# Kernel optimization log

Measured on AMD Instinct MI355X. Metric: run time of the kernel, lower is better.

The kernel has to match this reference:

```python
import jax, jax.numpy as jnp
import numpy as np

D_MODEL = 768
NUM_HEAD = 12
D_K = D_MODEL // NUM_HEAD
NEG_BIG = -1e9


def setup_inputs() -> dict:
    key = jax.random.key(0)
    ks = jax.random.split(key, 16)
    B, S, D = 16, 512, D_MODEL
    scale = 1.0 / np.sqrt(D)
    inp = {
        "q": jax.random.normal(ks[0], (B, S, D), jnp.float32),
        "k": jax.random.normal(ks[1], (B, S, D), jnp.float32),
        "v": jax.random.normal(ks[2], (B, S, D), jnp.float32),
        # padding mask: 1 where masked, broadcast over heads and query dim
        "mask": jax.random.randint(ks[3], (B, 1, 1, S), 0, 2).astype(jnp.float32),
        # adjacency bias broadcast over heads
        "adj": jax.random.uniform(ks[4], (B, 1, S, S), jnp.float32),
        "Wq": jax.random.normal(ks[5], (D, D), jnp.float32) * scale,
        "bq": jnp.zeros((D,), jnp.float32),
        "Wk": jax.random.normal(ks[6], (D, D), jnp.float32) * scale,
        "bk": jnp.zeros((D,), jnp.float32),
        "Wv": jax.random.normal(ks[7], (D, D), jnp.float32) * scale,
        "bv": jnp.zeros((D,), jnp.float32),
        "Wo": jax.random.normal(ks[8], (D, D), jnp.float32) * scale,
        "bo": jnp.zeros((D,), jnp.float32),
    }
    return inp


def reference(q, k, v, mask, adj, Wq, bq, Wk, bk, Wv, bv, Wo, bo):
    B, S, D = q.shape
    H, dk = NUM_HEAD, D_K

    def proj(x, W, b):
        # nn.Linear: x @ W.T + b, then split heads -> [B, H, S, dk]
        y = jnp.einsum('bsd,ed->bse', x, W) + b
        return y.reshape(B, S, H, dk).transpose(0, 2, 1, 3)

    qh = proj(q, Wq, bq)
    kh = proj(k, Wk, bk)
    vh = proj(v, Wv, bv)

    scores = jnp.einsum('bhqd,bhkd->bhqk', qh, kh) / jnp.sqrt(jnp.float32(dk))
    scores = scores + mask * NEG_BIG + adj  # broadcast over heads
    attn = jax.nn.softmax(scores, axis=-1)
    x = jnp.einsum('bhqk,bhkd->bhqd', attn, vh)
    x = x.transpose(0, 2, 1, 3).reshape(B, S, D)
    return jnp.einsum('bsd,ed->bse', x, Wo) + bo
```

## Files before the change

### kernel.cpp

```cpp
#include <hip/hip_runtime.h>
#include <hip/hip_bf16.h>

#define SEQ 512
#define DM 768
#define NH 12
#define DK 64
#define NB 16
#define WN (DM * DM)
#define HE ((size_t)NB * SEQ * DM)

typedef __attribute__((ext_vector_type(8))) _Float16 f16x8;
typedef __attribute__((ext_vector_type(4))) float f32x4;

static __device__ __forceinline__ void gload16(const void* g, void* lds) {
    __builtin_amdgcn_global_load_lds(
        (const __attribute__((address_space(1))) unsigned int*)g,
        (__attribute__((address_space(3))) unsigned int*)lds, 16, 0, 0);
}

__global__ __launch_bounds__(256) void convert_w(
    const float* __restrict__ Wq, const float* __restrict__ Wk,
    const float* __restrict__ Wv, const float* __restrict__ Wo,
    _Float16* __restrict__ dst)
{
    size_t i8 = ((size_t)blockIdx.x * 256 + threadIdx.x) * 8;
    unsigned int s = (unsigned int)(i8 / WN);
    const float* src = s == 0 ? Wq : s == 1 ? Wk : s == 2 ? Wv : Wo;
    size_t off = i8 - (size_t)s * WN;
    float4 a = *(const float4*)(src + off);
    float4 b = *(const float4*)(src + off + 4);
    f16x8 h;
    h[0] = (_Float16)a.x; h[1] = (_Float16)a.y; h[2] = (_Float16)a.z; h[3] = (_Float16)a.w;
    h[4] = (_Float16)b.x; h[5] = (_Float16)b.y; h[6] = (_Float16)b.z; h[7] = (_Float16)b.w;
    *(f16x8*)(dst + i8) = h;
}

__global__ __launch_bounds__(256) void proj_qkv(
    const float* __restrict__ Aq, const float* __restrict__ Ak,
    const float* __restrict__ Av, const _Float16* __restrict__ Wh,
    const float* __restrict__ bq, const float* __restrict__ bk, const float* __restrict__ bv,
    _Float16* __restrict__ P1, _Float16* __restrict__ P2, _Float16* __restrict__ P3)
{
    __shared__ float As[128][64];
    __shared__ _Float16 Bs[128][64];
    const int f = blockIdx.x;
    const int lg = (f & 7) * 144 + (f >> 3);
    const int sel = lg / 384;
    const int rem = lg - sel * 384;
    const int bm = (rem / 6) * 128, bn = (rem % 6) * 128;
    const float* A = sel == 0 ? Aq : sel == 1 ? Ak : Av;
    const _Float16* W = Wh + (size_t)sel * WN;
    const float* bias = sel == 0 ? bq : sel == 1 ? bk : bv;
    _Float16* O = sel == 0 ? P1 : sel == 1 ? P2 : P3;

    const int t = threadIdx.x, lane = t & 63, w = t >> 6;
    const int wm = w >> 1, wn = w & 1, g = lane >> 4, r16 = lane & 15;

    const int ar4 = lane >> 4, agr = lane & 15;
    const int br8 = lane >> 3, bgr = lane & 7;

    f32x4 acc[4][4] = {};

    const _Float16* gbs = W + (size_t)(bn + w * 32 + br8) * DM + ((bgr ^ br8) * 8);

    for (int kk = 0; kk < DM; kk += 64) {
        #pragma unroll
        for (int j = 0; j < 8; ++j) {
            const int row = w * 32 + j * 4 + ar4;
            const int gg  = (agr & 8) + ((agr & 7) ^ (row & 7));
            gload16(A + (size_t)(bm + row) * DM + kk + gg * 4, &As[w * 32 + j * 4][0]);
        }
        #pragma unroll
        for (int j = 0; j < 4; ++j)
            gload16(gbs + kk + (size_t)j * 8 * DM, &Bs[w * 32 + j * 8][0]);
        __syncthreads();
        #pragma unroll
        for (int h = 0; h < 2; ++h) {
            f16x8 af[4], bf[4];
            #pragma unroll
            for (int mi = 0; mi < 4; ++mi) {
                const int row = wm * 64 + mi * 16 + r16;
                const int p0 = h * 8 + ((2 * g)     ^ (r16 & 7));
                const int p1 = h * 8 + ((2 * g + 1) ^ (r16 & 7));
                f32x4 x0 = *(f32x4*)&As[row][p0 * 4];
                f32x4 x1 = *(f32x4*)&As[row][p1 * 4];
                f16x8 hh;
                hh[0] = (_Float16)x0[0]; hh[1] = (_Float16)x0[1];
                hh[2] = (_Float16)x0[2]; hh[3] = (_Float16)x0[3];
                hh[4] = (_Float16)x1[0]; hh[5] = (_Float16)x1[1];
                hh[6] = (_Float16)x1[2]; hh[7] = (_Float16)x1[3];
                af[mi] = hh;
            }
            #pragma unroll
            for (int ni = 0; ni < 4; ++ni)
                bf[ni] = *(f16x8*)&Bs[wn * 64 + ni * 16 + r16][(((h * 4 + g) ^ (r16 & 7))) * 8];
            #pragma unroll
            for (int mi = 0; mi < 4; ++mi)
                #pragma unroll
                for (int ni = 0; ni < 4; ++ni)
                    acc[mi][ni] = __builtin_amdgcn_mfma_f32_16x16x32_f16(af[mi], bf[ni], acc[mi][ni], 0, 0, 0);
        }
        __syncthreads();
    }
    #pragma unroll
    for (int ni = 0; ni < 4; ++ni) {
        int n = bn + wn * 64 + ni * 16 + r16;
        float bv_ = bias[n];
        #pragma unroll
        for (int mi = 0; mi < 4; ++mi) {
            #pragma unroll
            for (int r = 0; r < 4; ++r) {
                int m = bm + wm * 64 + mi * 16 + g * 4 + r;
                O[(size_t)m * DM + n] = (_Float16)(acc[mi][ni][r] + bv_);
            }
        }
    }
}

__global__ __launch_bounds__(256) void proj_o(
    const _Float16* __restrict__ A, const _Float16* __restrict__ W,
    const float* __restrict__ bias, float* __restrict__ O32)
{
    __shared__ _Float16 As[128][64];
    __shared__ _Float16 Bs[128][64];
    const int f = blockIdx.x;
    const int lg = (f & 7) * 48 + (f >> 3);
    const int bm = (lg / 6) * 128, bn = (lg % 6) * 128;
    const int t = threadIdx.x, lane = t & 63, w = t >> 6;
    const int wm = w >> 1, wn = w & 1, g = lane >> 4, r16 = lane & 15;
    const int br8 = lane >> 3, bgr = lane & 7;

    f32x4 acc[4][4] = {};

    const _Float16* gas = A + (size_t)(bm + w * 32 + br8) * DM + ((bgr ^ br8) * 8);
    const _Float16* gbs = W + (size_t)(bn + w * 32 + br8) * DM + ((bgr ^ br8) * 8);

    for (int kk = 0; kk < DM; kk += 64) {
        #pragma unroll
        for (int j = 0; j < 4; ++j) {
            gload16(gas + kk + (size_t)j * 8 * DM, &As[w * 32 + j * 8][0]);
            gload16(gbs + kk + (size_t)j * 8 * DM, &Bs[w * 32 + j * 8][0]);
        }
        __syncthreads();
        #pragma unroll
        for (int h = 0; h < 2; ++h) {
            f16x8 af[4], bf[4];
            #pragma unroll
            for (int mi = 0; mi < 4; ++mi)
                af[mi] = *(f16x8*)&As[wm * 64 + mi * 16 + r16][((h * 4 + g) ^ (r16 & 7)) * 8];
            #pragma unroll
            for (int ni = 0; ni < 4; ++ni)
                bf[ni] = *(f16x8*)&Bs[wn * 64 + ni * 16 + r16][((h * 4 + g) ^ (r16 & 7)) * 8];
            #pragma unroll
            for (int mi = 0; mi < 4; ++mi)
                #pragma unroll
                for (int ni = 0; ni < 4; ++ni)
                    acc[mi][ni] = __builtin_amdgcn_mfma_f32_16x16x32_f16(af[mi], bf[ni], acc[mi][ni], 0, 0, 0);
        }
        __syncthreads();
    }
    #pragma unroll
    for (int ni = 0; ni < 4; ++ni) {
        int n = bn + wn * 64 + ni * 16 + r16;
        float bv_ = bias[n];
        #pragma unroll
        for (int mi = 0; mi < 4; ++mi) {
            #pragma unroll
            for (int r = 0; r < 4; ++r) {
                int m = bm + wm * 64 + mi * 16 + g * 4 + r;
                O32[(size_t)m * DM + n] = acc[mi][ni][r] + bv_;
            }
        }
    }
}

#define VSWI(d, kcol) ((d) * 72 + ((((kcol) * 2) ^ ((((d) >> 3) & 7) << 4)) >> 1))
__global__ __launch_bounds__(256) void attn(
    const _Float16* __restrict__ Qp, const _Float16* __restrict__ Kp,
    const _Float16* __restrict__ Vp, const float* __restrict__ Adj,
    const float* __restrict__ Mask, _Float16* __restrict__ X)
{
    __shared__ _Float16 Ks[2][64 * 64];
    __shared__ _Float16 Vt[2][64 * 72];
    __shared__ _Float16 Ps[4][16][72];
    const int id = blockIdx.x;
    const int lid = (id & 7) * 192 + (id >> 3);
    const int h = lid % NH, qb = (lid / NH) & 7, b = lid / (NH * 8);
    const int t = threadIdx.x, lane = t & 63, w = t >> 6;
    const int g = lane >> 4, r16 = lane & 15;
    const int srow = t >> 2, sc = (t & 3) * 16;

    const _Float16* Qg = Qp + (size_t)(b * SEQ + qb * 64 + w * 16 + r16) * DM + h * DK;
    const f16x8 qf0 = *(const f16x8*)(Qg + g * 8);
    const f16x8 qf1 = *(const f16x8*)(Qg + 32 + g * 8);

    const _Float16* Kbh   = Kp + (size_t)(b * SEQ) * DM + h * DK;
    const _Float16* Vbase = Vp + (size_t)(b * SEQ) * DM + h * DK + sc;
    const float* Abase = Adj + ((size_t)b << 18)
                             + (size_t)(qb * 64 + w * 16 + g * 4) * SEQ + r16;
    const float* Mbase = Mask + ((size_t)b << 9) + r16;

    uint4 vv[2];
    float am[16];
    float mtv[4];

#define STAGEK(KB, BUF) { _Pragma("unroll") for (int j_ = 0; j_ < 2; ++j_) { \
        const _Float16* src_ = Kbh + (size_t)((KB) * 64 + w * 16 + j_ * 8 + (lane >> 3)) * DM \
                              + (((lane & 7) ^ (lane >> 3)) * 8); \
        gload16(src_, &Ks[BUF][(w * 16 + j_ * 8) * 64]); } }
#define LOADV(KB) { const _Float16* vp_ = Vbase + (size_t)((KB) * 64 + srow) * DM; \
        vv[0] = ((const uint4*)vp_)[0]; vv[1] = ((const uint4*)vp_)[1]; }
#define LOADA(KB) { _Pragma("unroll") for (int r = 0; r < 4; ++r) \
        _Pragma("unroll") for (int cb = 0; cb < 4; ++cb) \
            am[r * 4 + cb] = Abase[(size_t)r * SEQ + (KB) * 64 + cb * 16]; \
        _Pragma("unroll") for (int cb = 0; cb < 4; ++cb) \
            mtv[cb] = Mbase[(KB) * 64 + cb * 16]; }

    STAGEK(0, 0);
    __builtin_amdgcn_sched_barrier(0);
    LOADV(0);
    LOADA(0);

    float l_lane[4] = {0.f, 0.f, 0.f, 0.f};
    f32x4 o[4] = {};

    #pragma unroll
    for (int kb = 0; kb < 8; ++kb) {
        const int buf = kb & 1;
        {
            union { uint4 u[2]; _Float16 hh[16]; } cv;
            cv.u[0] = vv[0]; cv.u[1] = vv[1];
            _Float16* vt = &Vt[buf][0];
            #pragma unroll
            for (int i = 0; i < 16; ++i) vt[VSWI(sc + i, srow)] = cv.hh[i];
        }
        asm volatile("s_waitcnt lgkmcnt(0)" ::: "memory");
        __builtin_amdgcn_sched_barrier(0);
        __builtin_amdgcn_s_barrier();
        __builtin_amdgcn_sched_barrier(0);

        f32x4 sf[4] = {};
        __builtin_amdgcn_s_setprio(1);
        #pragma unroll
        for (int cb = 0; cb < 4; ++cb) {
            const int R = cb * 16 + r16;
            f16x8 k0 = *(f16x8*)&Ks[buf][R * 64 + ((g ^ (r16 & 7)) * 8)];
            f16x8 k1 = *(f16x8*)&Ks[buf][R * 64 + (((4 + g) ^ (r16 & 7)) * 8)];
            sf[cb] = __builtin_amdgcn_mfma_f32_16x16x32_f16(qf0, k0, sf[cb], 0, 0, 0);
            sf[cb] = __builtin_amdgcn_mfma_f32_16x16x32_f16(qf1, k1, sf[cb], 0, 0, 0);
        }
        __builtin_amdgcn_s_setprio(0);
        if (kb < 7) {
            STAGEK(kb + 1, buf ^ 1);
            __builtin_amdgcn_sched_barrier(0);
            LOADV(kb + 1);
        }
        #pragma unroll
        for (int cb = 0; cb < 4; ++cb) {
            const float term = fmaf(mtv[cb], -43280.8512f, -11.54156036f);
            #pragma unroll
            for (int r = 0; r < 4; ++r) {
                float e = exp2f(fmaf(sf[cb][r], 0.18033688f,
                            fmaf(am[r * 4 + cb], 1.44269504f, term)));
                sf[cb][r] = e;
                l_lane[r] += e;
            }
        }
        if (kb < 7) LOADA(kb + 1);
        #pragma unroll
        for (int cb = 0; cb < 4; ++cb)
            #pragma unroll
            for (int r = 0; r < 4; ++r)
                Ps[w][g * 4 + r][cb * 16 + r16] = (_Float16)sf[cb][r];
        __builtin_amdgcn_s_setprio(1);
        #pragma unroll
        for (int ks = 0; ks < 2; ++ks) {
            f16x8 pf = *(f16x8*)&Ps[w][r16][ks * 32 + g * 8];
            #pragma unroll
            for (int db = 0; db < 4; ++db) {
                f16x8 vf = *(f16x8*)&Vt[buf][VSWI(db * 16 + r16, ks * 32 + g * 8)];
                o[db] = __builtin_amdgcn_mfma_f32_16x16x32_f16(pf, vf, o[db], 0, 0, 0);
            }
        }
        __builtin_amdgcn_s_setprio(0);
    }
#undef STAGEK
#undef LOADV
#undef LOADA
    #pragma unroll
    for (int d = 1; d < 16; d <<= 1)
        #pragma unroll
        for (int r = 0; r < 4; ++r)
            l_lane[r] += __shfl_xor(l_lane[r], d);
    const int qrow = qb * 64 + w * 16 + g * 4;
    #pragma unroll
    for (int r = 0; r < 4; ++r) {
        float inv = 1.f / l_lane[r];
        _Float16* xp = X + (size_t)(b * SEQ + qrow + r) * DM + h * DK;
        #pragma unroll
        for (int db = 0; db < 4; ++db)
            xp[db * 16 + r16] = (_Float16)(o[db][r] * inv);
    }
}

extern "C" void kernel_launch(void* const* d_in, const int* in_sizes, int n_in,
                              void* d_out, int out_size, void* d_ws, size_t ws_size,
                              hipStream_t stream)
{
    const float* q    = (const float*)d_in[0];
    const float* k    = (const float*)d_in[1];
    const float* v    = (const float*)d_in[2];
    const float* mask = (const float*)d_in[3];
    const float* adj  = (const float*)d_in[4];
    const float* Wq   = (const float*)d_in[5];
    const float* bq   = (const float*)d_in[6];
    const float* Wk   = (const float*)d_in[7];
    const float* bk   = (const float*)d_in[8];
    const float* Wv   = (const float*)d_in[9];
    const float* bv   = (const float*)d_in[10];
    const float* Wo   = (const float*)d_in[11];
    const float* bo   = (const float*)d_in[12];
    float* out = (float*)d_out;

    _Float16* Wh = (_Float16*)d_ws;
    _Float16* P1 = Wh + 4 * WN;
    _Float16* P2 = P1 + HE;
    _Float16* P3 = P2 + HE;
    _Float16* X  = P3 + HE;

    convert_w<<<dim3(1152), dim3(256), 0, stream>>>(Wq, Wk, Wv, Wo, Wh);
    proj_qkv<<<dim3(1152), dim3(256), 0, stream>>>(q, k, v, Wh, bq, bk, bv, P1, P2, P3);
    attn<<<dim3(1536), dim3(256), 0, stream>>>(P1, P2, P3, adj, mask, X);
    proj_o<<<dim3(384), dim3(256), 0, stream>>>(X, Wh + 3 * WN, bo, out);
}
```

Baseline: 110.3 us.

## Read QKV activations directly from global and double-buffer weight tiles in LDS

The fp32 activation tile is no longer staged through shared memory. Each lane loads its A fragments straight from global memory and converts them to fp16 in registers. The weight tile is double-buffered in LDS, with the next tile prefetched while the current one is used, so there is one barrier per iteration instead of two. This frees 32KB of LDS per block and overlaps weight loads with compute. The cost is uncoalesced direct global reads of A, which two wave columns fetch redundantly, with latency exposed right before the MFMAs.

```diff
diff --git a/kernel.cpp b/kernel.cpp
--- a/kernel.cpp
+++ b/kernel.cpp
@@ -41,8 +41,7 @@
     const float* __restrict__ bq, const float* __restrict__ bk, const float* __restrict__ bv,
     _Float16* __restrict__ P1, _Float16* __restrict__ P2, _Float16* __restrict__ P3)
 {
-    __shared__ float As[128][64];
-    __shared__ _Float16 Bs[128][64];
+    __shared__ _Float16 Bs[2][128][64];
     const int f = blockIdx.x;
     const int lg = (f & 7) * 144 + (f >> 3);
     const int sel = lg / 384;
@@ -55,35 +54,33 @@
 
     const int t = threadIdx.x, lane = t & 63, w = t >> 6;
     const int wm = w >> 1, wn = w & 1, g = lane >> 4, r16 = lane & 15;
-
-    const int ar4 = lane >> 4, agr = lane & 15;
     const int br8 = lane >> 3, bgr = lane & 7;
 
     f32x4 acc[4][4] = {};
 
     const _Float16* gbs = W + (size_t)(bn + w * 32 + br8) * DM + ((bgr ^ br8) * 8);
-
-    for (int kk = 0; kk < DM; kk += 64) {
-        #pragma unroll
-        for (int j = 0; j < 8; ++j) {
-            const int row = w * 32 + j * 4 + ar4;
-            const int gg  = (agr & 8) + ((agr & 7) ^ (row & 7));
-            gload16(A + (size_t)(bm + row) * DM + kk + gg * 4, &As[w * 32 + j * 4][0]);
-        }
-        #pragma unroll
-        for (int j = 0; j < 4; ++j)
-            gload16(gbs + kk + (size_t)j * 8 * DM, &Bs[w * 32 + j * 8][0]);
-        __syncthreads();
+    const float* gar[4];
+    #pragma unroll
+    for (int mi = 0; mi < 4; ++mi)
+        gar[mi] = A + (size_t)(bm + wm * 64 + mi * 16 + r16) * DM + g * 8;
+
+#define STAGEB(KK, BUF) { _Pragma("unroll") for (int j = 0; j < 4; ++j) \
+        gload16(gbs + (KK) + (size_t)j * 8 * DM, &Bs[BUF][w * 32 + j * 8][0]); }
+
+    STAGEB(0, 0);
+    __syncthreads();
+
+    for (int tt = 0; tt < 12; ++tt) {
+        const int buf = tt & 1;
+        const int kk = tt * 64;
+        if (tt < 11) STAGEB(kk + 64, buf ^ 1);
         #pragma unroll
         for (int h = 0; h < 2; ++h) {
             f16x8 af[4], bf[4];
             #pragma unroll
             for (int mi = 0; mi < 4; ++mi) {
-                const int row = wm * 64 + mi * 16 + r16;
-                const int p0 = h * 8 + ((2 * g)     ^ (r16 & 7));
-                const int p1 = h * 8 + ((2 * g + 1) ^ (r16 & 7));
-                f32x4 x0 = *(f32x4*)&As[row][p0 * 4];
-                f32x4 x1 = *(f32x4*)&As[row][p1 * 4];
+                f32x4 x0 = *(const f32x4*)(gar[mi] + kk + h * 32);
+                f32x4 x1 = *(const f32x4*)(gar[mi] + kk + h * 32 + 4);
                 f16x8 hh;
                 hh[0] = (_Float16)x0[0]; hh[1] = (_Float16)x0[1];
                 hh[2] = (_Float16)x0[2]; hh[3] = (_Float16)x0[3];
@@ -93,7 +90,7 @@
             }
             #pragma unroll
             for (int ni = 0; ni < 4; ++ni)
-                bf[ni] = *(f16x8*)&Bs[wn * 64 + ni * 16 + r16][(((h * 4 + g) ^ (r16 & 7))) * 8];
+                bf[ni] = *(f16x8*)&Bs[buf][wn * 64 + ni * 16 + r16][((h * 4 + g) ^ (r16 & 7)) * 8];
             #pragma unroll
             for (int mi = 0; mi < 4; ++mi)
                 #pragma unroll
@@ -102,6 +99,8 @@
         }
         __syncthreads();
     }
+#undef STAGEB
+
     #pragma unroll
     for (int ni = 0; ni < 4; ++ni) {
         int n = bn + wn * 64 + ni * 16 + r16;
```

Result: slower. 191.7 us (+73.9%).
